# Optimization experiments

Hardware: AMD Instinct MI355X
Metric: run time of the kernel (lower is better)

## Reference

```python
import jax, jax.numpy as jnp
import numpy as np

T, N, C, D, S = 512, 32, 1296, 512, 30
NORM_SCALE = 32.0
NEGINF = -1e9


def setup_inputs() -> dict:
    key = jax.random.key(0)
    k1, k2, k3, k4, k5 = jax.random.split(key, 5)
    feats = jax.random.normal(k1, (T * N, D), dtype=jnp.float32)
    classifier_weight = jax.random.normal(k2, (D, C), dtype=jnp.float32)
    labeling = jax.random.randint(k3, (N, S), 1, C)  # targets cannot be blank(0)
    logit_lgts = (T - jax.random.randint(k4, (N,), 0, 32)).astype(jnp.int32)
    labeling_lgts = (S - jax.random.randint(k5, (N,), 0, 5)).astype(jnp.int32)
    return dict(feats=feats, classifier_weight=classifier_weight,
                labeling=labeling, logit_lgts=logit_lgts, labeling_lgts=labeling_lgts)


def _ctc_loss(log_probs, labels, in_lens, lab_lens):
    # log_probs: (T, N, C); labels: (N, S); blank = 0; reduction = 'sum'
    Tt, Nn, Cc = log_probs.shape
    Ss = labels.shape[1]
    L = 2 * Ss + 1
    # extended labeling: blank, l1, blank, l2, ..., blank  -> (N, L)
    ext = jnp.zeros((Nn, L), dtype=labels.dtype).at[:, 1::2].set(labels)
    # gather per-state log-probs: (T, N, L)
    lp_ext = jnp.take_along_axis(log_probs, jnp.broadcast_to(ext[None], (Tt, Nn, L)), axis=2)
    # skip transition s-2 -> s allowed iff s > 1 and ext[s] != ext[s-2]
    skip_ok = jnp.concatenate(
        [jnp.zeros((Nn, 2), dtype=bool), ext[:, 2:] != ext[:, :-2]], axis=1)
    alpha0 = (jnp.full((Nn, L), NEGINF, dtype=log_probs.dtype)
              .at[:, 0].set(lp_ext[0, :, 0])
              .at[:, 1].set(lp_ext[0, :, 1]))

    def step(alpha, inp):
        lp_t, t = inp  # lp_t: (N, L)
        a1 = alpha
        a2 = jnp.pad(alpha[:, :-1], ((0, 0), (1, 0)), constant_values=NEGINF)
        a3 = jnp.where(skip_ok,
                       jnp.pad(alpha[:, :-2], ((0, 0), (2, 0)), constant_values=NEGINF),
                       NEGINF)
        new = jax.nn.logsumexp(jnp.stack([a1, a2, a3], axis=0), axis=0) + lp_t
        # freeze alpha once t reaches a sample's input length
        alpha = jnp.where((t < in_lens)[:, None], new, alpha)
        return alpha, None

    alpha, _ = jax.lax.scan(step, alpha0, (lp_ext[1:], jnp.arange(1, Tt)))
    Ln = 2 * lab_lens + 1  # (N,)
    last = jnp.take_along_axis(alpha, (Ln - 1)[:, None], axis=1)[:, 0]
    last2 = jnp.take_along_axis(alpha, (Ln - 2)[:, None], axis=1)[:, 0]
    nll = -jnp.logaddexp(last, last2)
    return jnp.sum(nll)


def reference(feats, classifier_weight, labeling, logit_lgts, labeling_lgts):
    # RadialCTC: cosine logits with norm_scale, then CTC on log-softmax.
    w_n = classifier_weight / jnp.linalg.norm(classifier_weight, axis=0, keepdims=True)  # (D, C)
    f_n = feats / jnp.linalg.norm(feats, axis=1, keepdims=True)  # (T*N, D)
    logits = NORM_SCALE * (f_n @ w_n)  # (T*N, C)
    log_probs = jax.nn.log_softmax(logits.reshape(T, N, C), axis=-1)
    return _ctc_loss(log_probs, labeling, logit_lgts, labeling_lgts)
```

## Files before the change

### kernel.cpp

```cpp
#include <hip/hip_runtime.h>
#include <stdint.h>
#include <stddef.h>


typedef _Float16 f16;
typedef _Float16 f16x8 __attribute__((ext_vector_type(8)));
typedef float f32x4 __attribute__((ext_vector_type(4)));
typedef __attribute__((address_space(1))) void* as1_void_ptr;
typedef __attribute__((address_space(3))) void* as3_void_ptr;

#define TT 512
#define NN 32
#define CC 1296
#define DD 512
#define SS 30
#define CP 1408
#define LL 61
#define NORM_SCALE 32.0f
#define LOG2E 1.4426950408889634f
#define LN2   0.6931471805599453f

#define PREP_WBLK (CP / 16)
#define PREP_ZBLK 16
#define PREP_FBLK (TT * NN / 4)

#define GEMM_BLK ((TT * NN / 128) * (CP / 128))
#define MEGA_GC  NN
#define MEGA_BLK (MEGA_GC + GEMM_BLK)

__device__ __forceinline__ float fexp2(float x) { return __builtin_amdgcn_exp2f(x); }
__device__ __forceinline__ float flog2(float x) { return __builtin_amdgcn_logf(x); }

__device__ __forceinline__ double dpp_sr1_zero64(double x) {
    long long b = __double_as_longlong(x);
    int lo = (int)(b & 0xFFFFFFFFLL);
    int hi = (int)(b >> 32);
    int lo2 = __builtin_amdgcn_update_dpp(0, lo, 0x138, 0xF, 0xF, false);
    int hi2 = __builtin_amdgcn_update_dpp(0, hi, 0x138, 0xF, 0xF, false);
    return __longlong_as_double(((long long)hi2 << 32) |
                                (unsigned long long)(unsigned int)lo2);
}
template <int CTRL>
__device__ __forceinline__ int dpp_imax_level(int m) {
    int t = __builtin_amdgcn_update_dpp(0, m, CTRL, 0xF, 0xF, false);
    return m > t ? m : t;
}

__global__ __launch_bounds__(256) void prep_kernel(const float* __restrict__ W,
                                                   const float* __restrict__ feats,
                                                   f16* __restrict__ wt,
                                                   f16* __restrict__ fn,
                                                   float* __restrict__ sumexp) {
    int bx = blockIdx.x, tid = threadIdx.x;
    if (bx < PREP_WBLK) {
        __shared__ float red[256];
        __shared__ float rqs[16];
        int c0 = bx * 16;
        int cl = tid & 15, dg = tid >> 4;
        int c = c0 + cl;
        float ss = 0.f;
        if (c < CC) {
            for (int d = dg; d < DD; d += 16) {
                float v = W[(size_t)d * CC + c];
                ss += v * v;
            }
        }
        red[tid] = ss;
        __syncthreads();
        if (tid < 16) {
            float s2 = 0.f;
            #pragma unroll
            for (int k = 0; k < 16; ++k) s2 += red[tid + 16 * k];
            rqs[tid] = rsqrtf(s2);
        }
        __syncthreads();
        int c_loc = tid >> 4, dl = tid & 15;
        int cc = c0 + c_loc;
        float rq = rqs[c_loc];
        #pragma unroll 4
        for (int it = 0; it < 32; ++it) {
            int d = dl + it * 16;
            float v = (cc < CC) ? W[(size_t)d * CC + cc] * rq : 0.f;
            wt[(size_t)cc * DD + d] = (f16)v;
        }
    } else if (bx < PREP_WBLK + PREP_ZBLK) {
        int zb = bx - PREP_WBLK;
        float4 z = {0.f, 0.f, 0.f, 0.f};
        ((float4*)sumexp)[zb * 256 + tid] = z;
    } else {
        int fb = bx - PREP_WBLK - PREP_ZBLK;
        int wv = (fb * 256 + tid) >> 6;
        int lane = tid & 63;
        const float4* src = (const float4*)(feats + (size_t)wv * DD) + lane * 2;
        float4 a = src[0], b = src[1];
        float ss = a.x*a.x + a.y*a.y + a.z*a.z + a.w*a.w
                 + b.x*b.x + b.y*b.y + b.z*b.z + b.w*b.w;
        #pragma unroll
        for (int off = 32; off; off >>= 1) ss += __shfl_xor(ss, off);
        float r = rsqrtf(ss);
        f16x8 o;
        o[0]=(f16)(a.x*r); o[1]=(f16)(a.y*r); o[2]=(f16)(a.z*r); o[3]=(f16)(a.w*r);
        o[4]=(f16)(b.x*r); o[5]=(f16)(b.y*r); o[6]=(f16)(b.z*r); o[7]=(f16)(b.w*r);
        *(f16x8*)(fn + (size_t)wv * DD + lane * 8) = o;
    }
}

__global__ __launch_bounds__(256) void mega_kernel(const f16* __restrict__ A,
                                                   const f16* __restrict__ B,
                                                   const int* __restrict__ labels,
                                                   const int* __restrict__ in_lens,
                                                   const int* __restrict__ lab_lens,
                                                   float* __restrict__ sumexp,
                                                   float* __restrict__ lp_lab,
                                                   double* __restrict__ part) {
    __shared__ __align__(16) f16 sm[9216];
    int bx = blockIdx.x;
    int tid = threadIdx.x;
    int w = tid >> 6, lane = tid & 63;
    int lm = lane & 15, hi = lane >> 4;
    int sw = (lm >> 1) & 3;

    if (bx >= MEGA_GC) {
        int j = bx - MEGA_GC;
        int bm = j & 127, bn = j >> 7;
        int wm = w >> 1, wn = w & 1;
        f32x4 acc[4][4];
        f32x4 zero = {0.f, 0.f, 0.f, 0.f};
        #pragma unroll
        for (int i = 0; i < 4; ++i)
            #pragma unroll
            for (int jj = 0; jj < 4; ++jj) acc[i][jj] = zero;

        for (int kb = 0; kb < 16; ++kb) {
            #pragma unroll
            for (int p = 0; p < 2; ++p) {
                int s = p * 256 + tid;
                int row = s >> 2;
                int ch = (s & 3) ^ ((row >> 1) & 3);
                const f16* ga = A + (size_t)(bm * 128 + row) * DD + kb * 32 + ch * 8;
                const f16* gb = B + (size_t)(bn * 128 + row) * DD + kb * 32 + ch * 8;
                __builtin_amdgcn_global_load_lds((as1_void_ptr)ga,
                    (as3_void_ptr)&sm[(p * 256 + w * 64) * 8], 16, 0, 0);
                __builtin_amdgcn_global_load_lds((as1_void_ptr)gb,
                    (as3_void_ptr)&sm[4096 + (p * 256 + w * 64) * 8], 16, 0, 0);
            }
            __syncthreads();
            f16x8 af[4], bf[4];
            #pragma unroll
            for (int i = 0; i < 4; ++i)
                af[i] = *(const f16x8*)&sm[(wm * 64 + i * 16 + lm) * 32 + (hi ^ sw) * 8];
            #pragma unroll
            for (int jj = 0; jj < 4; ++jj)
                bf[jj] = *(const f16x8*)&sm[4096 + (wn * 64 + jj * 16 + lm) * 32 + (hi ^ sw) * 8];
            #pragma unroll
            for (int i = 0; i < 4; ++i)
                #pragma unroll
                for (int jj = 0; jj < 4; ++jj)
                    acc[i][jj] = __builtin_amdgcn_mfma_f32_16x16x32_f16(af[i], bf[jj], acc[i][jj], 0, 0, 0);
            __syncthreads();
        }
        #pragma unroll
        for (int i = 0; i < 4; ++i) {
            float rs[4] = {0.f, 0.f, 0.f, 0.f};
            #pragma unroll
            for (int jj = 0; jj < 4; ++jj) {
                int c = bn * 128 + wn * 64 + jj * 16 + lm;
                bool ok = (c < CC);
                #pragma unroll
                for (int r = 0; r < 4; ++r)
                    rs[r] += ok ? fexp2(acc[i][jj][r] * (NORM_SCALE * LOG2E)) : 0.f;
            }
            #pragma unroll
            for (int off = 1; off < 16; off <<= 1) {
                #pragma unroll
                for (int r = 0; r < 4; ++r) rs[r] += __shfl_xor(rs[r], off);
            }
            if (lm == 0) {
                int rowb = bm * 128 + wm * 64 + i * 16 + hi * 4;
                #pragma unroll
                for (int r = 0; r < 4; ++r) atomicAdd(&sumexp[rowb + r], rs[r]);
            }
        }
        return;
    }

    int n = bx;
    int brow = tid >> 2;
    int bch = (tid & 3) ^ ((brow >> 1) & 3);
    int cls = (brow == 0 || brow > SS) ? 0 : labels[n * SS + brow - 1];
    const f16* gbB = B + (size_t)cls * DD + bch * 8;

    for (int thalf = 0; thalf < 2; ++thalf) {
        int t0a = thalf * 256;
        f32x4 acc[4][2];
        #pragma unroll
        for (int i = 0; i < 4; ++i) {
            acc[i][0] = (f32x4){0.f, 0.f, 0.f, 0.f};
            acc[i][1] = (f32x4){0.f, 0.f, 0.f, 0.f};
        }
        for (int kb = 0; kb < 16; ++kb) {
            #pragma unroll
            for (int it = 0; it < 4; ++it) {
                int s = it * 256 + tid;
                int row = s >> 2;
                int ch = (s & 3) ^ ((row >> 1) & 3);
                const f16* ga = A + (size_t)((t0a + row) * NN + n) * DD + kb * 32 + ch * 8;
                __builtin_amdgcn_global_load_lds((as1_void_ptr)ga,
                    (as3_void_ptr)&sm[(it * 256 + w * 64) * 8], 16, 0, 0);
            }
            if (tid < 128)
                __builtin_amdgcn_global_load_lds((as1_void_ptr)(gbB + kb * 32),
                    (as3_void_ptr)&sm[8192 + (w * 64) * 8], 16, 0, 0);
            __syncthreads();
            f16x8 bf0 = *(const f16x8*)&sm[8192 + lm * 32 + (hi ^ sw) * 8];
            f16x8 bf1 = *(const f16x8*)&sm[8192 + (16 + lm) * 32 + (hi ^ sw) * 8];
            #pragma unroll
            for (int i = 0; i < 4; ++i) {
                f16x8 af = *(const f16x8*)&sm[(w * 64 + i * 16 + lm) * 32 + (hi ^ sw) * 8];
                acc[i][0] = __builtin_amdgcn_mfma_f32_16x16x32_f16(af, bf0, acc[i][0], 0, 0, 0);
                acc[i][1] = __builtin_amdgcn_mfma_f32_16x16x32_f16(af, bf1, acc[i][1], 0, 0, 0);
            }
            __syncthreads();
        }
        #pragma unroll
        for (int jn = 0; jn < 2; ++jn) {
            int jc = jn * 16 + lm;
            if (jc >= 31) continue;
            float* dst = lp_lab + ((size_t)n * 31 + jc) * TT + t0a;
            #pragma unroll
            for (int i = 0; i < 4; ++i)
                #pragma unroll
                for (int r = 0; r < 4; ++r)
                    dst[w * 64 + i * 16 + hi * 4 + r] = acc[i][jn][r] * (NORM_SCALE * LOG2E);
        }
    }
    __syncthreads();
    if (w != 0) return;

    int s = lane;
    bool valid = s < LL;
    int ext = (valid && (s & 1)) ? labels[n * SS + (s >> 1)] : 0;
    int jmap = (valid && (s & 1)) ? ((s >> 1) + 1) : 0;
    int ext2 = __shfl_up(ext, 2);
    double skipd = ((s >= 2) && valid && (ext != ext2)) ? 1.0 : 0.0;
    int Tin = in_lens[n];
    const float4* g0 = (const float4*)(lp_lab + ((size_t)n * 31 + jmap) * TT);

    float4 cur = g0[0];
    float4 nxt = g0[1];
    float4 nx2 = g0[2];
    double beta = (s <= 1) ? (double)fexp2(cur.x) : 0.0;
    int Mi = 0;

    auto stepL = [&](float lp) {
        double P = (double)fexp2(lp);
        double b1 = dpp_sr1_zero64(beta);
        double b2 = dpp_sr1_zero64(b1);
        beta = (beta + b1 + b2 * skipd) * P;
    };
    auto renorm = [&]() {
        int h = (int)(__double_as_longlong(beta) >> 32);
        h = dpp_imax_level<0x111>(h);
        h = dpp_imax_level<0x112>(h);
        h = dpp_imax_level<0x114>(h);
        h = dpp_imax_level<0x118>(h);
        int r0 = __builtin_amdgcn_readlane(h, 15);
        int r1 = __builtin_amdgcn_readlane(h, 31);
        int r2 = __builtin_amdgcn_readlane(h, 47);
        int r3 = __builtin_amdgcn_readlane(h, 63);
        int mx = max(max(r0, r1), max(r2, r3));
        int e11 = mx >> 20;
        double scale = __longlong_as_double((long long)(2046 - e11) << 52);
        beta *= scale;
        Mi += e11 - 1023;
    };

    stepL(cur.y); stepL(cur.z); stepL(cur.w);
    renorm();
    int remaining = Tin - 4;
    int g = 1;
    while (remaining >= 4) {
        cur = nxt; nxt = nx2;
        int gi = g + 2; if (gi > 127) gi = 127;
        nx2 = g0[gi];
        stepL(cur.x); stepL(cur.y); stepL(cur.z); stepL(cur.w);
        renorm();
        remaining -= 4; ++g;
    }
    cur = nxt;
    if (remaining > 0) stepL(cur.x);
    if (remaining > 1) stepL(cur.y);
    if (remaining > 2) stepL(cur.z);

    int Ln = 2 * lab_lens[n] + 1;
    double last  = __shfl(beta, Ln - 1);
    double last2 = __shfl(beta, Ln - 2);
    double smv = last + last2;
    long long bb = __double_as_longlong(smv);
    int e = (int)(bb >> 52) - 1023;
    double mant = __longlong_as_double((bb & 0xFFFFFFFFFFFFFLL) | (1023LL << 52));
    if (s == 0)
        part[n] = (double)flog2((float)mant) + (double)(e + Mi);
}

__global__ __launch_bounds__(1024) void final_kernel(const float* __restrict__ sumexp,
                                                     const int* __restrict__ in_lens,
                                                     const double* __restrict__ part,
                                                     float* __restrict__ out) {
    int tid = threadIdx.x;
    int v = tid >> 6, lane = tid & 63;
    __shared__ float nl[NN];
    #pragma unroll
    for (int k = 0; k < 2; ++k) {
        int n = v * 2 + k;
        int Tin = in_lens[n];
        double ms = 0.0;
        for (int t = lane; t < Tin; t += 64)
            ms += (double)flog2(sumexp[(size_t)t * NN + n]);
        #pragma unroll
        for (int off = 32; off; off >>= 1) ms += __shfl_xor(ms, off);
        if (lane == 0) nl[n] = (float)(-(part[n] - ms) * LN2);
    }
    __syncthreads();
    if (tid == 0) {
        float t = 0.f;
        for (int i = 0; i < NN; ++i) t += nl[i];
        out[0] = t;
    }
}

extern "C" void kernel_launch(void* const* d_in, const int* in_sizes, int n_in,
                              void* d_out, int out_size, void* d_ws, size_t ws_size,
                              hipStream_t stream) {
    const float* feats        = (const float*)d_in[0];
    const float* W            = (const float*)d_in[1];
    const int*   labeling     = (const int*)d_in[2];
    const int*   logit_lgts   = (const int*)d_in[3];
    const int*   labeling_lgts= (const int*)d_in[4];
    float* out = (float*)d_out;
    char* ws = (char*)d_ws;

    size_t off = 0;
    f16*   wt     = (f16*)(ws + off);   off += (size_t)CP * DD * 2;
    f16*   fn     = (f16*)(ws + off);   off += (size_t)TT * NN * DD * 2;
    float* sumexp = (float*)(ws + off); off += (size_t)TT * NN * 4;
    float* lp_lab = (float*)(ws + off); off += (size_t)NN * 31 * TT * 4;
    double* part  = (double*)(ws + off); off += NN * 8;

    prep_kernel<<<PREP_WBLK + PREP_ZBLK + PREP_FBLK, 256, 0, stream>>>(
        W, feats, wt, fn, sumexp);
    mega_kernel<<<MEGA_BLK, 256, 0, stream>>>(fn, wt, labeling, logit_lgts,
                                              labeling_lgts, sumexp, lp_lab, part);
    final_kernel<<<1, 1024, 0, stream>>>(sumexp, logit_lgts, part, out);

    (void)in_sizes; (void)n_in; (void)out_size; (void)ws_size;
}
```

Measured before the change: 159.0 us.

## Overlap per-sample label-gather GEMM with the CTC recursion in chunks

The per-sample block now splits its work across waves. Waves 1-3 compute the label-column logits for 128-timestep chunks, loading operands straight from global memory into MFMA instead of staging them through LDS. Wave 0 runs the CTC alpha recursion at the same time, waiting on a block barrier before consuming each new chunk. This hides the serial recursion behind the gather GEMM instead of running the two back to back. The cost is fewer waves doing the GEMM and uncoalesced direct global loads in place of LDS staging.

```diff
diff --git a/kernel.cpp b/kernel.cpp
--- a/kernel.cpp
+++ b/kernel.cpp
@@ -105,6 +105,55 @@
     }
 }
 
+template <int NT>
+__device__ __forceinline__ void gather_wave(const f16* __restrict__ A,
+                                            const f16* __restrict__ B,
+                                            const int* __restrict__ labels,
+                                            float* __restrict__ lp_lab,
+                                            int n, int rbase, int lane) {
+    int lm = lane & 15, hi = lane >> 4;
+    int cls0 = (lm == 0) ? 0 : labels[n * SS + lm - 1];
+    int cls1 = (lm >= 15) ? 0 : labels[n * SS + lm + 15];
+    const f16* pb0 = B + (size_t)cls0 * DD + hi * 8;
+    const f16* pb1 = B + (size_t)cls1 * DD + hi * 8;
+    const f16* pa0 = A + ((size_t)(rbase + lm) * NN + n) * DD + hi * 8;
+    for (int c = 0; c < 4; ++c) {
+        f32x4 acc[NT][2];
+        #pragma unroll
+        for (int i = 0; i < NT; ++i) {
+            acc[i][0] = (f32x4){0.f, 0.f, 0.f, 0.f};
+            acc[i][1] = (f32x4){0.f, 0.f, 0.f, 0.f};
+        }
+        const f16* pac = pa0 + (size_t)c * 128 * NN * DD;
+        for (int kb = 0; kb < 16; ++kb) {
+            f16x8 bf0 = *(const f16x8*)(pb0 + kb * 32);
+            f16x8 bf1 = *(const f16x8*)(pb1 + kb * 32);
+            #pragma unroll
+            for (int i = 0; i < NT; ++i) {
+                f16x8 af = *(const f16x8*)(pac + (size_t)(i * 16) * NN * DD + kb * 32);
+                acc[i][0] = __builtin_amdgcn_mfma_f32_16x16x32_f16(af, bf0, acc[i][0], 0, 0, 0);
+                acc[i][1] = __builtin_amdgcn_mfma_f32_16x16x32_f16(af, bf1, acc[i][1], 0, 0, 0);
+            }
+        }
+        #pragma unroll
+        for (int i = 0; i < NT; ++i) {
+            #pragma unroll
+            for (int jn = 0; jn < 2; ++jn) {
+                int jc = jn * 16 + lm;
+                if (jc >= 31) continue;
+                float4 o;
+                o.x = acc[i][jn][0] * (NORM_SCALE * LOG2E);
+                o.y = acc[i][jn][1] * (NORM_SCALE * LOG2E);
+                o.z = acc[i][jn][2] * (NORM_SCALE * LOG2E);
+                o.w = acc[i][jn][3] * (NORM_SCALE * LOG2E);
+                *(float4*)&lp_lab[((size_t)n * 31 + jc) * TT
+                                  + c * 128 + rbase + i * 16 + hi * 4] = o;
+            }
+        }
+        __syncthreads();
+    }
+}
+
 __global__ __launch_bounds__(256) void mega_kernel(const f16* __restrict__ A,
                                                    const f16* __restrict__ B,
                                                    const int* __restrict__ labels,
@@ -113,7 +162,7 @@
                                                    float* __restrict__ sumexp,
                                                    float* __restrict__ lp_lab,
                                                    double* __restrict__ part) {
-    __shared__ __align__(16) f16 sm[9216];
+    __shared__ __align__(16) f16 sm[8192];
     int bx = blockIdx.x;
     int tid = threadIdx.x;
     int w = tid >> 6, lane = tid & 63;
@@ -185,57 +234,11 @@
     }
 
     int n = bx;
-    int brow = tid >> 2;
-    int bch = (tid & 3) ^ ((brow >> 1) & 3);
-    int cls = (brow == 0 || brow > SS) ? 0 : labels[n * SS + brow - 1];
-    const f16* gbB = B + (size_t)cls * DD + bch * 8;
-
-    for (int thalf = 0; thalf < 2; ++thalf) {
-        int t0a = thalf * 256;
-        f32x4 acc[4][2];
-        #pragma unroll
-        for (int i = 0; i < 4; ++i) {
-            acc[i][0] = (f32x4){0.f, 0.f, 0.f, 0.f};
-            acc[i][1] = (f32x4){0.f, 0.f, 0.f, 0.f};
-        }
-        for (int kb = 0; kb < 16; ++kb) {
-            #pragma unroll
-            for (int it = 0; it < 4; ++it) {
-                int s = it * 256 + tid;
-                int row = s >> 2;
-                int ch = (s & 3) ^ ((row >> 1) & 3);
-                const f16* ga = A + (size_t)((t0a + row) * NN + n) * DD + kb * 32 + ch * 8;
-                __builtin_amdgcn_global_load_lds((as1_void_ptr)ga,
-                    (as3_void_ptr)&sm[(it * 256 + w * 64) * 8], 16, 0, 0);
-            }
-            if (tid < 128)
-                __builtin_amdgcn_global_load_lds((as1_void_ptr)(gbB + kb * 32),
-                    (as3_void_ptr)&sm[8192 + (w * 64) * 8], 16, 0, 0);
-            __syncthreads();
-            f16x8 bf0 = *(const f16x8*)&sm[8192 + lm * 32 + (hi ^ sw) * 8];
-            f16x8 bf1 = *(const f16x8*)&sm[8192 + (16 + lm) * 32 + (hi ^ sw) * 8];
-            #pragma unroll
-            for (int i = 0; i < 4; ++i) {
-                f16x8 af = *(const f16x8*)&sm[(w * 64 + i * 16 + lm) * 32 + (hi ^ sw) * 8];
-                acc[i][0] = __builtin_amdgcn_mfma_f32_16x16x32_f16(af, bf0, acc[i][0], 0, 0, 0);
-                acc[i][1] = __builtin_amdgcn_mfma_f32_16x16x32_f16(af, bf1, acc[i][1], 0, 0, 0);
-            }
-            __syncthreads();
-        }
-        #pragma unroll
-        for (int jn = 0; jn < 2; ++jn) {
-            int jc = jn * 16 + lm;
-            if (jc >= 31) continue;
-            float* dst = lp_lab + ((size_t)n * 31 + jc) * TT + t0a;
-            #pragma unroll
-            for (int i = 0; i < 4; ++i)
-                #pragma unroll
-                for (int r = 0; r < 4; ++r)
-                    dst[w * 64 + i * 16 + hi * 4 + r] = acc[i][jn][r] * (NORM_SCALE * LOG2E);
-        }
-    }
-    __syncthreads();
-    if (w != 0) return;
+    if (w > 0) {
+        if (w < 3) gather_wave<3>(A, B, labels, lp_lab, n, (w - 1) * 48, lane);
+        else       gather_wave<2>(A, B, labels, lp_lab, n, 96, lane);
+        return;
+    }
 
     int s = lane;
     bool valid = s < LL;
@@ -244,11 +247,12 @@
     int ext2 = __shfl_up(ext, 2);
     double skipd = ((s >= 2) && valid && (ext != ext2)) ? 1.0 : 0.0;
     int Tin = in_lens[n];
-    const float4* g0 = (const float4*)(lp_lab + ((size_t)n * 31 + jmap) * TT);
-
-    float4 cur = g0[0];
-    float4 nxt = g0[1];
-    float4 nx2 = g0[2];
+    const float4* g4 = (const float4*)(lp_lab + ((size_t)n * 31 + jmap) * TT);
+
+    __syncthreads();
+    float4 cur = g4[0];
+    float4 nxt = g4[1];
+    float4 nx2 = g4[2];
     double beta = (s <= 1) ? (double)fexp2(cur.x) : 0.0;
     int Mi = 0;
 
@@ -279,13 +283,21 @@
     renorm();
     int remaining = Tin - 4;
     int g = 1;
-    while (remaining >= 4) {
-        cur = nxt; nxt = nx2;
-        int gi = g + 2; if (gi > 127) gi = 127;
-        nx2 = g0[gi];
-        stepL(cur.x); stepL(cur.y); stepL(cur.z); stepL(cur.w);
-        renorm();
-        remaining -= 4; ++g;
+    for (int c = 0; c < 4; ++c) {
+        if (c > 0) {
+            __syncthreads();
+            nxt = g4[g];
+            nx2 = g4[g + 1];
+        }
+        int gend = 32 * (c + 1);
+        while (g < gend && remaining >= 4) {
+            cur = nxt; nxt = nx2;
+            int gi = g + 2; if (gi > 127) gi = 127;
+            nx2 = g4[gi];
+            stepL(cur.x); stepL(cur.y); stepL(cur.z); stepL(cur.w);
+            renorm();
+            remaining -= 4; ++g;
+        }
     }
     cur = nxt;
     if (remaining > 0) stepL(cur.x);
```

Result: slower. 163.1 us (+2.6%).
